# Kernel tuning notes

Hardware: AMD Instinct MI355X
Metric: run time of the kernel (lower is better)

Reference implementation:

```python
import jax, jax.numpy as jnp
import numpy as np

# --- cfg constants (from init_kwargs) ---
T = 100
DT_MS = 1.0
MAX_RATE_HZ = 200.0
TAU_MEM = 20.0
TAU_PRE = 20.0
TAU_POST = 20.0
V_TH = 16.0
LR_POST = 0.01
LR_PRE = 0.012
W_MAX = 1.0
B, F, N_IN = 256, 1024, 784


def setup_inputs() -> dict:
    key = jax.random.key(0)
    k1, k2, k3 = jax.random.split(key, 3)
    image = jax.random.uniform(k1, (B, 1, 28, 28), dtype=jnp.float32)
    noise = jax.random.uniform(k2, (T, B, 1, 28, 28), dtype=jnp.float32)
    # non-negative excitatory weights, kernel 28x28 flattened -> (F, 784)
    W = jax.random.uniform(k3, (F, N_IN), dtype=jnp.float32) * 0.3
    return {"image": image, "W": W, "noise": noise}


def reference(image, W, noise):
    """Returns spike_count: (B, n_filters)."""
    b = image.shape[0]
    f = W.shape[0]
    # Poisson encoding: P(spike at t) = rate*dt = image * max_rate_hz * dt_ms/1000
    p = image.reshape(b, -1) * (MAX_RATE_HZ * DT_MS / 1000.0)        # (B, 784)
    spikes_in = (noise.reshape(T, b, -1) < p[None]).astype(jnp.float32)  # (T, B, 784)

    decay_mem = jnp.float32(np.exp(-DT_MS / TAU_MEM))
    decay_pre = jnp.float32(np.exp(-DT_MS / TAU_PRE))
    decay_post = jnp.float32(np.exp(-DT_MS / TAU_POST))

    def step(carry, pre):
        mem, w, apre, apost, cnt = carry
        # conv with 28x28 kernel, padding 0 == FC: (B,784) @ (784,F)
        I = pre @ w.T                                   # (B, F)
        mem = mem * decay_mem + I
        spk = (mem >= V_TH).astype(mem.dtype)           # LIF threshold
        mem = mem * (1.0 - spk)                         # reset to 0 on spike
        # --- STDP (pair-based, batch-averaged, Diehl & Cook style) ---
        apre = apre * decay_pre + pre                   # (B, 784) pre trace
        dw_plus = (LR_POST / b) * jnp.einsum('bf,bi->fi', spk, apre)   # LTP on post spike
        dw_minus = (LR_PRE / b) * jnp.einsum('bf,bi->fi', apost, pre)  # LTD on pre spike
        w = jnp.clip(w + dw_plus - dw_minus, 0.0, W_MAX)
        apost = apost * decay_post + spk                # (B, F) post trace
        cnt = cnt + spk
        return (mem, w, apre, apost, cnt), None

    init = (jnp.zeros((b, f), jnp.float32),   # mem
            W,                                 # plastic weights
            jnp.zeros((b, N_IN), jnp.float32), # apre
            jnp.zeros((b, f), jnp.float32),    # apost
            jnp.zeros((b, f), jnp.float32))    # spike_count
    (mem, w, apre, apost, cnt), _ = jax.lax.scan(step, init, spikes_in)
    return cnt
```

## Files before the change

kernel.cpp:

```cpp
#include <hip/hip_runtime.h>
#include <math.h>

#define TSTEPS 100
#define BB 256
#define FF 1024
#define NIN 784
#define NW 13
#define FW (FF / 64)
#define CAPA 192
#define CAPB 128

typedef unsigned long long u64;

__global__ __launch_bounds__(256) void k_init(
    const float* __restrict__ W, float* __restrict__ wT,
    float* __restrict__ mem, float* __restrict__ apre_rep, float* __restrict__ apost,
    u64* __restrict__ spkbits, u64* __restrict__ spkT, float* __restrict__ out)
{
    int idx = blockIdx.x * 256 + threadIdx.x;
    {
        int f = idx & (FF - 1);
        int i = idx >> 10;
        wT[idx] = W[f * NIN + i];
    }
    apre_rep[idx] = 0.f;
    apre_rep[idx + NIN * FF] = 0.f;
    if (idx < BB * FF)  { mem[idx] = 0.f; apost[idx] = 0.f; out[idx] = 0.f; }
    if (idx < BB * FW)  spkbits[idx] = 0ull;
    if (idx < 2 * FF * 4) spkT[idx] = 0ull;
}

__global__ __launch_bounds__(256) void k_encode(
    const float* __restrict__ image, const float* __restrict__ noise,
    u64* __restrict__ prebits)
{
    int tid = blockIdx.x * 256 + threadIdx.x;
    int lane = threadIdx.x & 63;
    int word = tid >> 6;
    int wd = word % NW;
    int tb = word / NW;
    int b = tb & (BB - 1);
    int i = (wd << 6) + lane;
    bool s = false;
    if (i < NIN) {
        float pf = __fmul_rn(image[b * NIN + i], 0.2f);
        s = (noise[(size_t)tb * NIN + i] < pf);
    }
    u64 m = __ballot(s);
    if (lane == 0) prebits[word] = m;
}

__global__ __launch_bounds__(256) void k_encode_t(
    const u64* __restrict__ prebits, u64* __restrict__ prebitsT)
{
    int tid = blockIdx.x * 256 + threadIdx.x;
    int b = tid & (BB - 1);
    int ti = tid >> 8;
    int i = ti % NIN;
    int t = ti / NIN;
    u64 w = prebits[((size_t)t * BB + b) * NW + (i >> 6)];
    bool s = (w >> (i & 63)) & 1ull;
    u64 m = __ballot(s);
    if ((threadIdx.x & 63) == 0)
        prebitsT[(size_t)ti * 4 + ((threadIdx.x >> 6) & 3)] = m;
}

__global__ __launch_bounds__(256) void k_lists(
    const u64* __restrict__ prebits, unsigned short* __restrict__ idxA,
    unsigned short* __restrict__ cntA)
{
    int tb = blockIdx.x * 256 + threadIdx.x;
    const u64* pb = prebits + (size_t)tb * NW;
    unsigned short* ia = idxA + (size_t)tb * CAPA;
    int n = 0, c1 = 0, c2 = 0;
    for (int wd = 0; wd < NW; ++wd) {
        u64 m = pb[wd];
        int boff = wd << 6;
        while (m) {
            int j = __builtin_ctzll(m); m &= m - 1;
            if (n < CAPA) ia[n] = (unsigned short)(boff + j);
            ++n;
        }
        if (wd == 5)  c1 = n;
        if (wd == 11) c2 = n;
    }
    if (n > CAPA) n = CAPA;
    if (c2 > n) c2 = n;
    if (c1 > c2) c1 = c2;
    cntA[tb * 4 + 0] = (unsigned short)c1;
    cntA[tb * 4 + 1] = (unsigned short)c2;
    cntA[tb * 4 + 2] = (unsigned short)n;
}

__global__ __launch_bounds__(256) void k_listsT(
    const u64* __restrict__ prebitsT, unsigned char* __restrict__ idxB,
    unsigned short* __restrict__ cntB)
{
    int ti = blockIdx.x * 256 + threadIdx.x;
    if (ti >= TSTEPS * NIN) return;
    const u64* pt = prebitsT + (size_t)ti * 4;
    unsigned char* ib = idxB + (size_t)ti * CAPB;
    int n = 0;
    for (int wb = 0; wb < 4; ++wb) {
        u64 m = pt[wb];
        int boff = wb << 6;
        while (m) {
            int j = __builtin_ctzll(m); m &= m - 1;
            if (n < CAPB) ib[n] = (unsigned char)(boff + j);
            ++n;
        }
    }
    cntB[ti] = (unsigned short)(n > CAPB ? CAPB : n);
}

__global__ __launch_bounds__(128) void k_step_a(
    int t, const float* __restrict__ wT, float* __restrict__ mem,
    float* __restrict__ apre_rep, float* __restrict__ apost,
    const u64* __restrict__ prebits,
    const unsigned short* __restrict__ idxA, const unsigned short* __restrict__ cntA,
    u64* __restrict__ spkbits, u64* __restrict__ spkT_cur, u64* __restrict__ spkT_nxt,
    float* __restrict__ out, float dmem, float dpre, float dpost)
{
    int bid = blockIdx.x;
    int g = bid & 7;
    int b = bid >> 3;
    int f = (g << 7) | threadIdx.x;
    int tid = (b << 10) | f;

    u64 psw = spkbits[tid >> 6];
    float spk_prev = (float)((psw >> (f & 63)) & 1ull);
    float apo = __fadd_rn(__fmul_rn(apost[tid], dpost), spk_prev);
    apost[tid] = apo;

    const unsigned short* ia = idxA + (size_t)(t * BB + b) * CAPA;
    const unsigned short* ca = cntA + (size_t)(t * BB + b) * 4;
    int c1 = ca[0], c2 = ca[1], c3 = ca[2];
    float I = 0.0f;
    int k = 0;
    {
        float c = 0.0f;
        #pragma unroll 4
        for (; k < c1; ++k) c = __fadd_rn(c, wT[((int)ia[k] << 10) + f]);
        I = __fadd_rn(I, c);
    }
    {
        float c = 0.0f;
        #pragma unroll 4
        for (; k < c2; ++k) c = __fadd_rn(c, wT[((int)ia[k] << 10) + f]);
        I = __fadd_rn(I, c);
    }
    {
        float c = 0.0f;
        #pragma unroll 4
        for (; k < c3; ++k) c = __fadd_rn(c, wT[((int)ia[k] << 10) + f]);
        I = __fadd_rn(I, c);
    }

    float mm = __fadd_rn(__fmul_rn(mem[tid], dmem), I);
    bool spk = (mm >= 16.0f);
    mem[tid] = spk ? 0.0f : mm;
    if (spk) {
        out[tid] += 1.0f;
        atomicOr(&spkT_cur[(f << 2) | (b >> 6)], 1ull << (b & 63));
    }
    u64 bal = __ballot(spk);
    if ((threadIdx.x & 63) == 0) spkbits[tid >> 6] = bal;
    if (threadIdx.x < 2) spkT_nxt[bid * 2 + threadIdx.x] = 0ull;

    float* ap = apre_rep + (size_t)g * (BB * NIN);
    for (int e = b * NIN + threadIdx.x; e < (b + 1) * NIN; e += 128) {
        int bb = e & (BB - 1), ii = e >> 8;
        u64 w = prebits[((size_t)t * BB + bb) * NW + (ii >> 6)];
        float pr = (float)((w >> (ii & 63)) & 1ull);
        ap[e] = __fadd_rn(__fmul_rn(ap[e], dpre), pr);
    }
}

__global__ __launch_bounds__(128) void k_step_b(
    int t, float* __restrict__ wT, const float* __restrict__ apre_rep,
    const float* __restrict__ apost,
    const unsigned char* __restrict__ idxB, const unsigned short* __restrict__ cntB,
    const u64* __restrict__ spkT_cur, float lrp, float lrm)
{
    int bid = blockIdx.x;
    int g = bid & 7;
    int i = bid >> 3;
    int f = (g << 7) | threadIdx.x;

    const unsigned char* ib = idxB + (size_t)(t * NIN + i) * CAPB;
    int cb = cntB[t * NIN + i];
    float Sm = 0.0f;
    #pragma unroll 4
    for (int k = 0; k < cb; ++k)
        Sm = __fadd_rn(Sm, apost[((int)ib[k] << 10) + f]);

    const u64* st = spkT_cur + (f << 2);
    const float* ar = apre_rep + (size_t)g * (BB * NIN) + (i << 8);
    float Sp = 0.0f;
    for (int wb = 0; wb < 4; ++wb) {
        u64 m = st[wb];
        while (m) {
            int j = __builtin_ctzll(m); m &= m - 1;
            Sp = __fadd_rn(Sp, ar[(wb << 6) + j]);
        }
    }
    int wi = (i << 10) | f;
    float w = wT[wi];
    w = __fadd_rn(w, __fmul_rn(lrp, Sp));
    w = __fsub_rn(w, __fmul_rn(lrm, Sm));
    w = fminf(fmaxf(w, 0.0f), 1.0f);
    wT[wi] = w;
}

extern "C" void kernel_launch(void* const* d_in, const int* in_sizes, int n_in,
                              void* d_out, int out_size, void* d_ws, size_t ws_size,
                              hipStream_t stream)
{
    const float* image = (const float*)d_in[0];
    const float* W     = (const float*)d_in[1];
    const float* noise = (const float*)d_in[2];
    float* out = (float*)d_out;

    char* p = (char*)d_ws;
    float* wT       = (float*)p; p += (size_t)NIN * FF * 4;
    float* mem      = (float*)p; p += (size_t)BB * FF * 4;
    float* apre_rep = (float*)p; p += (size_t)8 * BB * NIN * 4;
    float* apost    = (float*)p; p += (size_t)BB * FF * 4;
    u64* prebits    = (u64*)p;   p += (size_t)TSTEPS * BB * NW * 8;
    u64* prebitsT   = (u64*)p;   p += (size_t)TSTEPS * NIN * 4 * 8;
    u64* spkbits    = (u64*)p;   p += (size_t)BB * FW * 8;
    u64* spkT       = (u64*)p;   p += (size_t)2 * FF * 4 * 8;
    unsigned short* idxA = (unsigned short*)p; p += (size_t)TSTEPS * BB * CAPA * 2;
    unsigned short* cntA = (unsigned short*)p; p += (size_t)TSTEPS * BB * 4 * 2;
    unsigned char*  idxB = (unsigned char*)p;  p += (size_t)TSTEPS * NIN * CAPB;
    unsigned short* cntB = (unsigned short*)p; p += (size_t)TSTEPS * NIN * 2;

    float dmem = (float)exp(-1.0 / 20.0);
    float dpre = dmem, dpost = dmem;
    float lrp = (float)(0.01 / 256.0);
    float lrm = (float)(0.012 / 256.0);

    k_init<<<(NIN * FF) / 256, 256, 0, stream>>>(W, wT, mem, apre_rep, apost, spkbits, spkT, out);
    k_encode<<<(TSTEPS * BB * NW * 64) / 256, 256, 0, stream>>>(image, noise, prebits);
    k_encode_t<<<(TSTEPS * NIN * BB) / 256, 256, 0, stream>>>(prebits, prebitsT);
    k_lists<<<(TSTEPS * BB) / 256, 256, 0, stream>>>(prebits, idxA, cntA);
    k_listsT<<<(TSTEPS * NIN + 255) / 256, 256, 0, stream>>>(prebitsT, idxB, cntB);

    for (int t = 0; t < TSTEPS; ++t) {
        u64* cur = spkT + (size_t)(t & 1) * FF * 4;
        u64* nxt = spkT + (size_t)((t + 1) & 1) * FF * 4;
        k_step_a<<<BB * 8, 128, 0, stream>>>(
            t, wT, mem, apre_rep, apost, prebits, idxA, cntA,
            spkbits, cur, nxt, out, dmem, dpre, dpost);
        if (t < TSTEPS - 1)
            k_step_b<<<NIN * 8, 128, 0, stream>>>(
                t, wT, apre_rep, apost, idxB, cntB, cur, lrp, lrm);
    }
}
```

Measured before the change: 5.561 ms.

## Fuse per-timestep kernels into one persistent kernel with grid barriers

Replaces the roughly 200 per-timestep kernel launches with a single persistent kernel of 2048 blocks. A hierarchical atomic grid barrier separates the neuron-update phase from the weight-update phase. Membrane potential, post trace and spike count now live in registers instead of global memory, and the weight-update rows are spread across blocks. The change removes launch overhead and some global traffic. It relies on all 2048 blocks being co-resident (the 4-per-CU launch bound), otherwise the barrier deadlocks, and the barrier spin adds its own cost.

```diff
diff --git a/kernel.cpp b/kernel.cpp
--- a/kernel.cpp
+++ b/kernel.cpp
@@ -6,16 +6,16 @@
 #define FF 1024
 #define NIN 784
 #define NW 13
-#define FW (FF / 64)
 #define CAPA 192
 #define CAPB 128
+#define NBLK 2048
 
 typedef unsigned long long u64;
 
 __global__ __launch_bounds__(256) void k_init(
     const float* __restrict__ W, float* __restrict__ wT,
-    float* __restrict__ mem, float* __restrict__ apre_rep, float* __restrict__ apost,
-    u64* __restrict__ spkbits, u64* __restrict__ spkT, float* __restrict__ out)
+    float* __restrict__ apre_rep, u64* __restrict__ spkT,
+    unsigned* __restrict__ bar)
 {
     int idx = blockIdx.x * 256 + threadIdx.x;
     {
@@ -25,9 +25,8 @@
     }
     apre_rep[idx] = 0.f;
     apre_rep[idx + NIN * FF] = 0.f;
-    if (idx < BB * FF)  { mem[idx] = 0.f; apost[idx] = 0.f; out[idx] = 0.f; }
-    if (idx < BB * FW)  spkbits[idx] = 0ull;
     if (idx < 2 * FF * 4) spkT[idx] = 0ull;
+    if (idx < 1024) bar[idx] = 0u;
 }
 
 __global__ __launch_bounds__(256) void k_encode(
@@ -113,13 +112,41 @@
     cntB[ti] = (unsigned short)(n > CAPB ? CAPB : n);
 }
 
-__global__ __launch_bounds__(128) void k_step_a(
-    int t, const float* __restrict__ wT, float* __restrict__ mem,
-    float* __restrict__ apre_rep, float* __restrict__ apost,
+__device__ __forceinline__ void grid_bar(unsigned* bar, int bid, unsigned ep1)
+{
+    __syncthreads();
+    if (threadIdx.x == 0) {
+        int leaf = bid & 7;
+        __threadfence();
+        unsigned v = __hip_atomic_fetch_add(bar + leaf * 32, 1u,
+                        __ATOMIC_RELAXED, __HIP_MEMORY_SCOPE_AGENT);
+        if (v == 256u * ep1 - 1u) {
+            __threadfence();
+            unsigned r = __hip_atomic_fetch_add(bar + 256, 1u,
+                            __ATOMIC_RELAXED, __HIP_MEMORY_SCOPE_AGENT);
+            if (r == 8u * ep1 - 1u) {
+                __threadfence();
+                #pragma unroll
+                for (int x = 0; x < 8; ++x)
+                    __hip_atomic_store(bar + 512 + x * 32, ep1,
+                        __ATOMIC_RELAXED, __HIP_MEMORY_SCOPE_AGENT);
+            }
+        }
+        while (__hip_atomic_load(bar + 512 + leaf * 32,
+                   __ATOMIC_RELAXED, __HIP_MEMORY_SCOPE_AGENT) < ep1)
+            __builtin_amdgcn_s_sleep(8);
+        __threadfence();
+    }
+    __syncthreads();
+}
+
+__global__ __launch_bounds__(128, 4) void k_run(
+    float* __restrict__ wT, float* __restrict__ apre_rep, float* __restrict__ apost,
     const u64* __restrict__ prebits,
     const unsigned short* __restrict__ idxA, const unsigned short* __restrict__ cntA,
-    u64* __restrict__ spkbits, u64* __restrict__ spkT_cur, u64* __restrict__ spkT_nxt,
-    float* __restrict__ out, float dmem, float dpre, float dpost)
+    const unsigned char* __restrict__ idxB, const unsigned short* __restrict__ cntB,
+    u64* __restrict__ spkT, float* __restrict__ out, unsigned* __restrict__ bar,
+    float dmem, float dpre, float dpost, float lrp, float lrm)
 {
     int bid = blockIdx.x;
     int g = bid & 7;
@@ -127,89 +154,95 @@
     int f = (g << 7) | threadIdx.x;
     int tid = (b << 10) | f;
 
-    u64 psw = spkbits[tid >> 6];
-    float spk_prev = (float)((psw >> (f & 63)) & 1ull);
-    float apo = __fadd_rn(__fmul_rn(apost[tid], dpost), spk_prev);
-    apost[tid] = apo;
-
-    const unsigned short* ia = idxA + (size_t)(t * BB + b) * CAPA;
-    const unsigned short* ca = cntA + (size_t)(t * BB + b) * 4;
-    int c1 = ca[0], c2 = ca[1], c3 = ca[2];
-    float I = 0.0f;
-    int k = 0;
-    {
-        float c = 0.0f;
-        #pragma unroll 4
-        for (; k < c1; ++k) c = __fadd_rn(c, wT[((int)ia[k] << 10) + f]);
-        I = __fadd_rn(I, c);
-    }
-    {
-        float c = 0.0f;
-        #pragma unroll 4
-        for (; k < c2; ++k) c = __fadd_rn(c, wT[((int)ia[k] << 10) + f]);
-        I = __fadd_rn(I, c);
-    }
-    {
-        float c = 0.0f;
-        #pragma unroll 4
-        for (; k < c3; ++k) c = __fadd_rn(c, wT[((int)ia[k] << 10) + f]);
-        I = __fadd_rn(I, c);
-    }
-
-    float mm = __fadd_rn(__fmul_rn(mem[tid], dmem), I);
-    bool spk = (mm >= 16.0f);
-    mem[tid] = spk ? 0.0f : mm;
-    if (spk) {
-        out[tid] += 1.0f;
-        atomicOr(&spkT_cur[(f << 2) | (b >> 6)], 1ull << (b & 63));
-    }
-    u64 bal = __ballot(spk);
-    if ((threadIdx.x & 63) == 0) spkbits[tid >> 6] = bal;
-    if (threadIdx.x < 2) spkT_nxt[bid * 2 + threadIdx.x] = 0ull;
-
-    float* ap = apre_rep + (size_t)g * (BB * NIN);
-    for (int e = b * NIN + threadIdx.x; e < (b + 1) * NIN; e += 128) {
-        int bb = e & (BB - 1), ii = e >> 8;
-        u64 w = prebits[((size_t)t * BB + bb) * NW + (ii >> 6)];
-        float pr = (float)((w >> (ii & 63)) & 1ull);
-        ap[e] = __fadd_rn(__fmul_rn(ap[e], dpre), pr);
-    }
-}
-
-__global__ __launch_bounds__(128) void k_step_b(
-    int t, float* __restrict__ wT, const float* __restrict__ apre_rep,
-    const float* __restrict__ apost,
-    const unsigned char* __restrict__ idxB, const unsigned short* __restrict__ cntB,
-    const u64* __restrict__ spkT_cur, float lrp, float lrm)
-{
-    int bid = blockIdx.x;
-    int g = bid & 7;
-    int i = bid >> 3;
-    int f = (g << 7) | threadIdx.x;
-
-    const unsigned char* ib = idxB + (size_t)(t * NIN + i) * CAPB;
-    int cb = cntB[t * NIN + i];
-    float Sm = 0.0f;
-    #pragma unroll 4
-    for (int k = 0; k < cb; ++k)
-        Sm = __fadd_rn(Sm, apost[((int)ib[k] << 10) + f]);
-
-    const u64* st = spkT_cur + (f << 2);
-    const float* ar = apre_rep + (size_t)g * (BB * NIN) + (i << 8);
-    float Sp = 0.0f;
-    for (int wb = 0; wb < 4; ++wb) {
-        u64 m = st[wb];
-        while (m) {
-            int j = __builtin_ctzll(m); m &= m - 1;
-            Sp = __fadd_rn(Sp, ar[(wb << 6) + j]);
-        }
-    }
-    int wi = (i << 10) | f;
-    float w = wT[wi];
-    w = __fadd_rn(w, __fmul_rn(lrp, Sp));
-    w = __fsub_rn(w, __fmul_rn(lrm, Sm));
-    w = fminf(fmaxf(w, 0.0f), 1.0f);
-    wT[wi] = w;
+    float memv = 0.f, cntv = 0.f, apov = 0.f;
+    u64 prev_bal = 0ull;
+    unsigned ep = 1;
+
+    for (int t = 0; t < TSTEPS; ++t) {
+        u64* cur = spkT + (size_t)(t & 1) * FF * 4;
+        u64* nxt = spkT + (size_t)((t + 1) & 1) * FF * 4;
+
+        float spk_prev = (float)((prev_bal >> (threadIdx.x & 63)) & 1ull);
+        apov = __fadd_rn(__fmul_rn(apov, dpost), spk_prev);
+        apost[tid] = apov;
+
+        const unsigned short* ia = idxA + (size_t)(t * BB + b) * CAPA;
+        const unsigned short* ca = cntA + (size_t)(t * BB + b) * 4;
+        int c1 = ca[0], c2 = ca[1], c3 = ca[2];
+        float I = 0.0f;
+        int k = 0;
+        {
+            float c = 0.0f;
+            #pragma unroll 4
+            for (; k < c1; ++k) c = __fadd_rn(c, wT[((int)ia[k] << 10) + f]);
+            I = __fadd_rn(I, c);
+        }
+        {
+            float c = 0.0f;
+            #pragma unroll 4
+            for (; k < c2; ++k) c = __fadd_rn(c, wT[((int)ia[k] << 10) + f]);
+            I = __fadd_rn(I, c);
+        }
+        {
+            float c = 0.0f;
+            #pragma unroll 4
+            for (; k < c3; ++k) c = __fadd_rn(c, wT[((int)ia[k] << 10) + f]);
+            I = __fadd_rn(I, c);
+        }
+
+        float mm = __fadd_rn(__fmul_rn(memv, dmem), I);
+        bool spk = (mm >= 16.0f);
+        memv = spk ? 0.0f : mm;
+        if (spk) {
+            cntv += 1.0f;
+            atomicOr(&cur[(f << 2) | (b >> 6)], 1ull << (b & 63));
+        }
+        prev_bal = __ballot(spk);
+        if (threadIdx.x < 2) nxt[bid * 2 + threadIdx.x] = 0ull;
+
+        float* ap = apre_rep + (size_t)g * (BB * NIN);
+        for (int e = b * NIN + threadIdx.x; e < (b + 1) * NIN; e += 128) {
+            int bb = e & (BB - 1), ii = e >> 8;
+            u64 w = prebits[((size_t)t * BB + bb) * NW + (ii >> 6)];
+            float pr = (float)((w >> (ii & 63)) & 1ull);
+            ap[e] = __fadd_rn(__fmul_rn(ap[e], dpre), pr);
+        }
+
+        grid_bar(bar, bid, ep); ++ep;
+
+        if (t < TSTEPS - 1) {
+            u64 m0 = cur[(f << 2) | 0], m1 = cur[(f << 2) | 1];
+            u64 m2 = cur[(f << 2) | 2], m3 = cur[(f << 2) | 3];
+            for (int i = b; i < NIN; i += BB) {
+                const unsigned char* ib = idxB + (size_t)(t * NIN + i) * CAPB;
+                int cb = cntB[t * NIN + i];
+                float Sm = 0.0f;
+                #pragma unroll 4
+                for (int k2 = 0; k2 < cb; ++k2)
+                    Sm = __fadd_rn(Sm, apost[((int)ib[k2] << 10) + f]);
+                const float* ar = apre_rep + (size_t)g * (BB * NIN) + (i << 8);
+                float Sp = 0.0f;
+                u64 mm0 = m0;
+                while (mm0) { int j = __builtin_ctzll(mm0); mm0 &= mm0 - 1; Sp = __fadd_rn(Sp, ar[j]); }
+                u64 mm1 = m1;
+                while (mm1) { int j = __builtin_ctzll(mm1); mm1 &= mm1 - 1; Sp = __fadd_rn(Sp, ar[64 + j]); }
+                u64 mm2 = m2;
+                while (mm2) { int j = __builtin_ctzll(mm2); mm2 &= mm2 - 1; Sp = __fadd_rn(Sp, ar[128 + j]); }
+                u64 mm3 = m3;
+                while (mm3) { int j = __builtin_ctzll(mm3); mm3 &= mm3 - 1; Sp = __fadd_rn(Sp, ar[192 + j]); }
+
+                int wi = (i << 10) | f;
+                float w = wT[wi];
+                w = __fadd_rn(w, __fmul_rn(lrp, Sp));
+                w = __fsub_rn(w, __fmul_rn(lrm, Sm));
+                w = fminf(fmaxf(w, 0.0f), 1.0f);
+                wT[wi] = w;
+            }
+            grid_bar(bar, bid, ep); ++ep;
+        }
+    }
+
+    out[tid] = cntv;
 }
 
 extern "C" void kernel_launch(void* const* d_in, const int* in_sizes, int n_in,
@@ -223,37 +256,29 @@
 
     char* p = (char*)d_ws;
     float* wT       = (float*)p; p += (size_t)NIN * FF * 4;
-    float* mem      = (float*)p; p += (size_t)BB * FF * 4;
     float* apre_rep = (float*)p; p += (size_t)8 * BB * NIN * 4;
     float* apost    = (float*)p; p += (size_t)BB * FF * 4;
     u64* prebits    = (u64*)p;   p += (size_t)TSTEPS * BB * NW * 8;
     u64* prebitsT   = (u64*)p;   p += (size_t)TSTEPS * NIN * 4 * 8;
-    u64* spkbits    = (u64*)p;   p += (size_t)BB * FW * 8;
     u64* spkT       = (u64*)p;   p += (size_t)2 * FF * 4 * 8;
     unsigned short* idxA = (unsigned short*)p; p += (size_t)TSTEPS * BB * CAPA * 2;
     unsigned short* cntA = (unsigned short*)p; p += (size_t)TSTEPS * BB * 4 * 2;
     unsigned char*  idxB = (unsigned char*)p;  p += (size_t)TSTEPS * NIN * CAPB;
     unsigned short* cntB = (unsigned short*)p; p += (size_t)TSTEPS * NIN * 2;
+    unsigned* bar        = (unsigned*)p;       p += 1024 * 4;
 
     float dmem = (float)exp(-1.0 / 20.0);
     float dpre = dmem, dpost = dmem;
     float lrp = (float)(0.01 / 256.0);
     float lrm = (float)(0.012 / 256.0);
 
-    k_init<<<(NIN * FF) / 256, 256, 0, stream>>>(W, wT, mem, apre_rep, apost, spkbits, spkT, out);
+    k_init<<<(NIN * FF) / 256, 256, 0, stream>>>(W, wT, apre_rep, spkT, bar);
     k_encode<<<(TSTEPS * BB * NW * 64) / 256, 256, 0, stream>>>(image, noise, prebits);
     k_encode_t<<<(TSTEPS * NIN * BB) / 256, 256, 0, stream>>>(prebits, prebitsT);
     k_lists<<<(TSTEPS * BB) / 256, 256, 0, stream>>>(prebits, idxA, cntA);
     k_listsT<<<(TSTEPS * NIN + 255) / 256, 256, 0, stream>>>(prebitsT, idxB, cntB);
 
-    for (int t = 0; t < TSTEPS; ++t) {
-        u64* cur = spkT + (size_t)(t & 1) * FF * 4;
-        u64* nxt = spkT + (size_t)((t + 1) & 1) * FF * 4;
-        k_step_a<<<BB * 8, 128, 0, stream>>>(
-            t, wT, mem, apre_rep, apost, prebits, idxA, cntA,
-            spkbits, cur, nxt, out, dmem, dpre, dpost);
-        if (t < TSTEPS - 1)
-            k_step_b<<<NIN * 8, 128, 0, stream>>>(
-                t, wT, apre_rep, apost, idxB, cntB, cur, lrp, lrm);
-    }
-}
+    k_run<<<NBLK, 128, 0, stream>>>(
+        wT, apre_rep, apost, prebits, idxA, cntA, idxB, cntB,
+        spkT, out, bar, dmem, dpre, dpost, lrp, lrm);
+}
```

Result: slower. 20.90 ms (+275.8%).
